# Kernel optimization log

Measured on AMD Instinct MI355X. Metric: run time of the kernel, lower is better.

## Reference

```python
import jax, jax.numpy as jnp
import numpy as np

D_MODEL = 1024
N_HEADS = 16
HEAD_DIM = D_MODEL // N_HEADS  # 64
BATCH = 2
SEQ = 2048
THETA = 10000.0


def _rope_tables(theta, d_k, max_seq_len):
    # matches RoPE.__init__: d = theta**(2*arange(d_k//2)/d_k); t = s / d
    inv = theta ** (2.0 * jnp.arange(0, d_k // 2, dtype=jnp.float32) / d_k)  # [d_k//2]
    s = jnp.arange(max_seq_len, dtype=jnp.float32)[:, None]  # [S,1]
    t = s / inv[None, :]  # [S, d_k//2]
    return jnp.sin(t), jnp.cos(t)


def setup_inputs() -> dict:
    key = jax.random.key(0)
    ks = jax.random.split(key, 5)
    std = np.sqrt(2.0 / (D_MODEL + D_MODEL))
    x = jax.random.normal(ks[0], (BATCH, SEQ, D_MODEL), dtype=jnp.float32)
    Wq = jax.random.normal(ks[1], (D_MODEL, D_MODEL), dtype=jnp.float32) * std
    Wk = jax.random.normal(ks[2], (D_MODEL, D_MODEL), dtype=jnp.float32) * std
    Wv = jax.random.normal(ks[3], (D_MODEL, D_MODEL), dtype=jnp.float32) * std
    Wo = jax.random.normal(ks[4], (D_MODEL, D_MODEL), dtype=jnp.float32) * std
    token_positions = jnp.arange(SEQ, dtype=jnp.int64)
    rope_sin, rope_cos = _rope_tables(THETA, HEAD_DIM, SEQ)
    return {"x": x, "token_positions": token_positions, "Wq": Wq, "Wk": Wk,
            "Wv": Wv, "Wo": Wo, "rope_sin": rope_sin, "rope_cos": rope_cos}


def _apply_rope(x, sin, cos):
    # x: [B, H, S, d_k]; sin/cos: [S, d_k//2] (gathered by token_positions)
    x1 = x[..., ::2]
    x2 = x[..., 1::2]
    x_even = x1 * cos - x2 * sin
    x_odd = x1 * sin + x2 * cos
    # interleave back: stack on last dim then flatten
    return jnp.stack([x_even, x_odd], axis=-1).reshape(x.shape)


def reference(x, token_positions, Wq, Wk, Wv, Wo, rope_sin, rope_cos):
    b, s, _ = x.shape
    h, d = N_HEADS, HEAD_DIM

    def proj(W):
        y = jnp.einsum('oi,bsi->bso', W, x)
        return y.reshape(b, s, h, d).transpose(0, 2, 1, 3)  # [b, h, s, d]

    q = proj(Wq)
    k = proj(Wk)
    v = proj(Wv)

    sin = rope_sin[token_positions]  # [s, d//2]
    cos = rope_cos[token_positions]
    q = _apply_rope(q, sin, cos)
    k = _apply_rope(k, sin, cos)

    # causal scaled-dot-product attention (FlashAttention.apply(..., True))
    scale = 1.0 / jnp.sqrt(jnp.asarray(d, dtype=x.dtype))
    scores = jnp.einsum('bhqd,bhkd->bhqk', q, k) * scale
    causal = jnp.tril(jnp.ones((s, s), dtype=bool))
    scores = jnp.where(causal, scores, jnp.finfo(x.dtype).min)
    attn = jax.nn.softmax(scores, axis=-1)
    out = jnp.einsum('bhqk,bhkd->bhqd', attn, v)  # [b, h, s, d]
    out = out.transpose(0, 2, 1, 3).reshape(b, s, h * d)
    return jnp.einsum('oi,bsi->bso', Wo, out)
```

## Files before the change

kernel.cpp:

```cpp
#include <hip/hip_runtime.h>
#include <hip/hip_bf16.h>
#include <math.h>

#define BATCH   2
#define S_LEN   2048
#define DM      1024
#define NH      16
#define HD      64
#define MROWS   4096

typedef __hip_bfloat16 bf16;
typedef __attribute__((ext_vector_type(8))) short short8;
typedef __attribute__((ext_vector_type(4))) float float4v;

#define QSCALE 0.18033688011112043f

#define WC_VM0   0x0F70
#define WC_VM4   0x0F74
#define WC_VM6   0x0F76
#define WC_LGKM0 0xC07F

__device__ __forceinline__ short f2s(float x) {
    union { bf16 h; short s; } u; u.h = __float2bfloat16(x); return u.s;
}
__device__ __forceinline__ short8 load8(const void* p) {
    return *reinterpret_cast<const short8*>(p);
}
__device__ __forceinline__ void cvt8(const float* g, bf16* d) {
    float4v a = *reinterpret_cast<const float4v*>(g);
    float4v b = *reinterpret_cast<const float4v*>(g + 4);
    short8 r;
    r[0] = f2s(a[0]); r[1] = f2s(a[1]); r[2] = f2s(a[2]); r[3] = f2s(a[3]);
    r[4] = f2s(b[0]); r[5] = f2s(b[1]); r[6] = f2s(b[2]); r[7] = f2s(b[3]);
    *reinterpret_cast<short8*>(d) = r;
}
__device__ __forceinline__ void gll16(const void* g, void* l) {
    __builtin_amdgcn_global_load_lds(
        (const __attribute__((address_space(1))) unsigned int*)g,
        (__attribute__((address_space(3))) unsigned int*)l,
        16, 0, 0);
}
__device__ __forceinline__ unsigned pack2(float a, float b) {
    union { float f; unsigned u; } ua, ub;
    ua.f = a; ub.f = b;
    return ((ua.u + 0x8000u) >> 16) | ((ub.u + 0x8000u) & 0xFFFF0000u);
}

__global__ __launch_bounds__(256) void cvt_kernel(const float* __restrict__ x,
                                                  const float* __restrict__ wq,
                                                  const float* __restrict__ wk,
                                                  const float* __restrict__ wv,
                                                  const float* __restrict__ wo,
                                                  bf16* __restrict__ xb,
                                                  bf16* __restrict__ wqb,
                                                  bf16* __restrict__ wkb,
                                                  bf16* __restrict__ wvb,
                                                  bf16* __restrict__ wob) {
    const size_t i = ((size_t)blockIdx.x * 256 + threadIdx.x) * 8;
    const size_t NX = (size_t)MROWS * DM;
    const size_t NW = (size_t)DM * DM;
    if (i < NX)                { cvt8(x  + i,               xb  + i); }
    else if (i < NX + NW)      { cvt8(wq + (i - NX),        wqb + (i - NX)); }
    else if (i < NX + 2 * NW)  { cvt8(wk + (i - NX - NW),   wkb + (i - NX - NW)); }
    else if (i < NX + 3 * NW)  { cvt8(wv + (i - NX - 2*NW), wvb + (i - NX - 2*NW)); }
    else                       { cvt8(wo + (i - NX - 3*NW), wob + (i - NX - 3*NW)); }
}

__global__ __launch_bounds__(256) void qkv_gemm(const bf16* __restrict__ A,
                                                const bf16* __restrict__ Wqb,
                                                const bf16* __restrict__ Wkb,
                                                const bf16* __restrict__ Wvb,
                                                bf16* __restrict__ Qb, bf16* __restrict__ Kb,
                                                bf16* __restrict__ Vtb,
                                                const float* __restrict__ rsin,
                                                const float* __restrict__ rcos) {
    __shared__ short As[2][128 * 32];
    __shared__ short Bs[2][128 * 32];

    const int j    = threadIdx.x;
    const int w    = j >> 6;
    const int lane = j & 63;
    const int quad = lane >> 4;
    const int lid  = lane & 15;
    const int wm   = w & 1, wn = w >> 1;

    const int mb  = blockIdx.x * 128;
    const int sel = blockIdx.y >> 3;
    const int nb  = (blockIdx.y & 7) * 128;
    const bf16* W = (sel == 0) ? Wqb : (sel == 1) ? Wkb : Wvb;

    int sOff[2];
#pragma unroll
    for (int i = 0; i < 2; ++i) {
        const int idx = (i * 4 + w) * 64 + lane;
        const int r = idx >> 2;
        const int c = (idx & 3) ^ (r & 3) ^ ((r >> 2) & 3);
        sOff[i] = r * DM + c * 8;
    }
    const bf16* baseA = A + (size_t)mb * DM;
    const bf16* baseB = W + (size_t)nb * DM;

#pragma unroll
    for (int i = 0; i < 2; ++i) gll16(baseA + sOff[i], &As[0][(i * 4 + w) * 512]);
#pragma unroll
    for (int i = 0; i < 2; ++i) gll16(baseB + sOff[i], &Bs[0][(i * 4 + w) * 512]);

    int aRd[4], bRd[4];
#pragma unroll
    for (int t = 0; t < 4; ++t) {
        const int ra = wm * 64 + t * 16 + lid;
        aRd[t] = ra * 32 + ((quad ^ (ra & 3) ^ ((ra >> 2) & 3)) * 8);
        const int rb = wn * 64 + t * 16 + lid;
        bRd[t] = rb * 32 + ((quad ^ (rb & 3) ^ ((rb >> 2) & 3)) * 8);
    }

    float4v acc[4][4] = {};
#pragma unroll 2
    for (int it = 0; it < 32; ++it) {
        __builtin_amdgcn_s_barrier();
        if (it < 31) {
            const int k0 = (it + 1) * 32, b = (it + 1) & 1;
#pragma unroll
            for (int i = 0; i < 2; ++i) gll16(baseA + k0 + sOff[i], &As[b][(i * 4 + w) * 512]);
#pragma unroll
            for (int i = 0; i < 2; ++i) gll16(baseB + k0 + sOff[i], &Bs[b][(i * 4 + w) * 512]);
            __builtin_amdgcn_s_waitcnt(WC_VM4);
        } else {
            __builtin_amdgcn_s_waitcnt(WC_VM0);
        }
        __builtin_amdgcn_s_barrier();

        const short* as = As[it & 1];
        const short* bs = Bs[it & 1];
        short8 af[4], bfr[4];
#pragma unroll
        for (int mt = 0; mt < 4; ++mt) af[mt] = load8(&as[aRd[mt]]);
#pragma unroll
        for (int nt = 0; nt < 4; ++nt) bfr[nt] = load8(&bs[bRd[nt]]);
#pragma unroll
        for (int mt = 0; mt < 4; ++mt)
#pragma unroll
            for (int nt = 0; nt < 4; ++nt)
                acc[mt][nt] = __builtin_amdgcn_mfma_f32_16x16x32_bf16(af[mt], bfr[nt], acc[mt][nt], 0, 0, 0);
    }

#pragma unroll
    for (int mt = 0; mt < 4; ++mt) {
#pragma unroll
        for (int nt = 0; nt < 4; ++nt) {
            const int n = nb + wn * 64 + nt * 16 + lid;
            const int h = n >> 6, d = n & 63;
#pragma unroll
            for (int r = 0; r < 4; ++r) {
                const int m = mb + wm * 64 + mt * 16 + quad * 4 + r;
                const int s = m & (S_LEN - 1), bi = m >> 11;
                float val = acc[mt][nt][r];
                if (sel == 0) val *= QSCALE;
                float par = __shfl_xor(val, 1, 64);
                if (sel == 2) {
                    Vtb[(((size_t)bi * NH + h) * HD + d) * S_LEN + s] = __float2bfloat16(val);
                } else {
                    const float sn = rsin[s * 32 + (d >> 1)];
                    const float cs = rcos[s * 32 + (d >> 1)];
                    const float v = ((d & 1) == 0) ? val * cs - par * sn
                                                   : par * sn + val * cs;
                    bf16* dst = (sel == 0) ? Qb : Kb;
                    dst[(((size_t)bi * NH + h) * S_LEN + s) * HD + d] = __float2bfloat16(v);
                }
            }
        }
    }
}

__global__ __launch_bounds__(256) void out_gemm(const bf16* __restrict__ A,
                                                const bf16* __restrict__ W,
                                                float* __restrict__ out) {
    __shared__ short As[2][128 * 64];
    __shared__ short Bs[2][64 * 64];

    const int j    = threadIdx.x;
    const int w    = j >> 6;
    const int lane = j & 63;
    const int quad = lane >> 4;
    const int lid  = lane & 15;

    const int mb = blockIdx.x * 128;
    const int nb = blockIdx.y * 64;

    int aOff[4], bOff[2];
#pragma unroll
    for (int i = 0; i < 4; ++i) {
        const int idx = (i * 4 + w) * 64 + lane;
        const int r = idx >> 3, c = (idx & 7) ^ (r & 7);
        aOff[i] = r * DM + c * 8;
    }
#pragma unroll
    for (int i = 0; i < 2; ++i) {
        const int idx = (i * 4 + w) * 64 + lane;
        const int r = idx >> 3, c = (idx & 7) ^ (r & 7);
        bOff[i] = r * DM + c * 8;
    }
    const bf16* baseA = A + (size_t)mb * DM;
    const bf16* baseB = W + (size_t)nb * DM;

#pragma unroll
    for (int i = 0; i < 4; ++i) gll16(baseA + aOff[i], &As[0][(i * 4 + w) * 512]);
#pragma unroll
    for (int i = 0; i < 2; ++i) gll16(baseB + bOff[i], &Bs[0][(i * 4 + w) * 512]);

    float4v acc[2][4] = {};
#pragma unroll 2
    for (int it = 0; it < 16; ++it) {
        __builtin_amdgcn_s_barrier();
        if (it < 15) {
            const int k0 = (it + 1) * 64, b = (it + 1) & 1;
#pragma unroll
            for (int i = 0; i < 4; ++i) gll16(baseA + k0 + aOff[i], &As[b][(i * 4 + w) * 512]);
#pragma unroll
            for (int i = 0; i < 2; ++i) gll16(baseB + k0 + bOff[i], &Bs[b][(i * 4 + w) * 512]);
            __builtin_amdgcn_s_waitcnt(WC_VM6);
        } else {
            __builtin_amdgcn_s_waitcnt(WC_VM0);
        }
        __builtin_amdgcn_s_barrier();

        const short* as = As[it & 1];
        const short* bs = Bs[it & 1];
#pragma unroll
        for (int ks = 0; ks < 2; ++ks) {
            short8 af[2], bfr[4];
#pragma unroll
            for (int mt = 0; mt < 2; ++mt)
                af[mt] = load8(&as[(w * 32 + mt * 16 + lid) * 64 + (((ks * 4 + quad) ^ (lid & 7)) * 8)]);
#pragma unroll
            for (int nt = 0; nt < 4; ++nt)
                bfr[nt] = load8(&bs[(nt * 16 + lid) * 64 + (((ks * 4 + quad) ^ (lid & 7)) * 8)]);
#pragma unroll
            for (int mt = 0; mt < 2; ++mt)
#pragma unroll
                for (int nt = 0; nt < 4; ++nt)
                    acc[mt][nt] = __builtin_amdgcn_mfma_f32_16x16x32_bf16(af[mt], bfr[nt], acc[mt][nt], 0, 0, 0);
        }
    }

#pragma unroll
    for (int mt = 0; mt < 2; ++mt)
#pragma unroll
        for (int nt = 0; nt < 4; ++nt) {
            const int n = nb + nt * 16 + lid;
#pragma unroll
            for (int r = 0; r < 4; ++r) {
                const int m = mb + w * 32 + mt * 16 + quad * 4 + r;
                out[(size_t)m * DM + n] = acc[mt][nt][r];
            }
        }
}

__global__ __launch_bounds__(256) void flash6(const bf16* __restrict__ Q,
                                              const bf16* __restrict__ K,
                                              const bf16* __restrict__ Vt,
                                              bf16* __restrict__ att) {
    __shared__ short Ks[128 * 64];
    __shared__ short Vs[64 * 128];
    __shared__ short Pb[128 * 128];

    const int j    = threadIdx.x;
    const int w    = j >> 6;
    const int lane = j & 63;
    const int quad = lane >> 4;
    const int lid  = lane & 15;
    const int bh   = blockIdx.x;
    const int by   = blockIdx.y;
    const int qt   = (by < 8) ? (15 - by) : (by - 8);
    const int bi   = bh >> 4, h = bh & 15;
    const int qb   = qt * 128;

    const size_t bh_off = (size_t)bh * S_LEN * HD;
    const bf16* Qp = Q + bh_off;
    const bf16* Kp = K + bh_off;
    const bf16* Vp = Vt + bh_off;

    short8 aQ[2][2];
#pragma unroll
    for (int mm = 0; mm < 2; ++mm)
#pragma unroll
        for (int kf = 0; kf < 2; ++kf)
            aQ[mm][kf] = load8(Qp + (size_t)(qb + w * 32 + mm * 16 + lid) * HD + kf * 32 + quad * 8);

    int kOff[4], vOff[4];
#pragma unroll
    for (int i = 0; i < 4; ++i) {
        const int idx = (i * 4 + w) * 64 + lane;
        const int kr = idx >> 3, kc = (idx & 7) ^ (kr & 7);
        kOff[i] = kr * HD + kc * 8;
        const int vr = idx >> 4, vc = (idx & 15) ^ (vr & 15);
        vOff[i] = vr * S_LEN + vc * 8;
    }

    float4v accO[2][4] = {};
    float4v accS[2] = {};
    short8 ones;
#pragma unroll
    for (int t = 0; t < 8; ++t) ones[t] = (short)0x3F80;

    short8 kReg[4], vReg[4];
#pragma unroll
    for (int i = 0; i < 4; ++i) kReg[i] = load8(Kp + kOff[i]);
#pragma unroll
    for (int i = 0; i < 4; ++i) vReg[i] = load8(Vp + vOff[i]);

    const int nkt = qt + 1;
    for (int kti = 0; kti < nkt; ++kti) {
        __builtin_amdgcn_s_barrier();
#pragma unroll
        for (int i = 0; i < 4; ++i)
            *reinterpret_cast<short8*>(&Ks[(i * 4 + w) * 512 + lane * 8]) = kReg[i];
#pragma unroll
        for (int i = 0; i < 4; ++i)
            *reinterpret_cast<short8*>(&Vs[(i * 4 + w) * 512 + lane * 8]) = vReg[i];
        if (kti + 1 < nkt) {
            const int ktn = (kti + 1) * 128;
#pragma unroll
            for (int i = 0; i < 4; ++i) kReg[i] = load8(Kp + (size_t)ktn * HD + kOff[i]);
#pragma unroll
            for (int i = 0; i < 4; ++i) vReg[i] = load8(Vp + ktn + vOff[i]);
        }
        __builtin_amdgcn_s_waitcnt(WC_LGKM0);
        __builtin_amdgcn_s_barrier();

        const int kt = kti * 128;
        const bool diag = (kti == nkt - 1);

#pragma unroll
        for (int nt = 0; nt < 8; ++nt) {
            const int krow = nt * 16 + lid;
            short8 aK0 = load8(&Ks[krow * 64 + ((quad       ^ (lid & 7)) * 8)]);
            short8 aK1 = load8(&Ks[krow * 64 + (((4 + quad) ^ (lid & 7)) * 8)]);
#pragma unroll
            for (int mm = 0; mm < 2; ++mm) {
                float4v z = {};
                z = __builtin_amdgcn_mfma_f32_16x16x32_bf16(aK0, aQ[mm][0], z, 0, 0, 0);
                z = __builtin_amdgcn_mfma_f32_16x16x32_bf16(aK1, aQ[mm][1], z, 0, 0, 0);
                if (diag) {
                    const int qcol = qb + w * 32 + mm * 16 + lid;
#pragma unroll
                    for (int r = 0; r < 4; ++r)
                        if (kt + nt * 16 + quad * 4 + r > qcol) z[r] = -1e30f;
                }
                const float p0 = __builtin_amdgcn_exp2f(z[0]);
                const float p1 = __builtin_amdgcn_exp2f(z[1]);
                const float p2 = __builtin_amdgcn_exp2f(z[2]);
                const float p3 = __builtin_amdgcn_exp2f(z[3]);
                const int qrow = w * 32 + mm * 16 + lid;
                const int unit = (nt * 4 + quad) ^ ((lid & 7) * 2);
                uint2 pkd; pkd.x = pack2(p0, p1); pkd.y = pack2(p2, p3);
                *reinterpret_cast<uint2*>(&Pb[qrow * 128 + unit * 4]) = pkd;
            }
        }

        short8 aP[2][4];
#pragma unroll
        for (int mm = 0; mm < 2; ++mm) {
            const int qrow = w * 32 + mm * 16 + lid;
#pragma unroll
            for (int g = 0; g < 4; ++g) {
                const int u = (g * 8 + quad * 2) ^ ((lid & 7) * 2);
                aP[mm][g] = load8(&Pb[qrow * 128 + u * 4]);
                accS[mm] = __builtin_amdgcn_mfma_f32_16x16x32_bf16(aP[mm][g], ones, accS[mm], 0, 0, 0);
            }
        }
#pragma unroll
        for (int dt = 0; dt < 4; ++dt) {
#pragma unroll
            for (int g = 0; g < 4; ++g) {
                short8 bV = load8(&Vs[(dt * 16 + lid) * 128 + (((g * 4 + quad) ^ lid) * 8)]);
#pragma unroll
                for (int mm = 0; mm < 2; ++mm)
                    accO[mm][dt] = __builtin_amdgcn_mfma_f32_16x16x32_bf16(aP[mm][g], bV, accO[mm][dt], 0, 0, 0);
            }
        }
    }

#pragma unroll
    for (int mm = 0; mm < 2; ++mm) {
#pragma unroll
        for (int r = 0; r < 4; ++r) {
            const float inv = 1.0f / accS[mm][r];
            const int q = qb + w * 32 + mm * 16 + quad * 4 + r;
#pragma unroll
            for (int dt = 0; dt < 4; ++dt) {
                const int d = dt * 16 + lid;
                att[((size_t)bi * S_LEN + q) * DM + h * HD + d] =
                    __float2bfloat16(accO[mm][dt][r] * inv);
            }
        }
    }
}

extern "C" void kernel_launch(void* const* d_in, const int* in_sizes, int n_in,
                              void* d_out, int out_size, void* d_ws, size_t ws_size,
                              hipStream_t stream) {
    const float* x    = (const float*)d_in[0];
    const float* Wq   = (const float*)d_in[2];
    const float* Wk   = (const float*)d_in[3];
    const float* Wv   = (const float*)d_in[4];
    const float* Wo   = (const float*)d_in[5];
    const float* rsin = (const float*)d_in[6];
    const float* rcos = (const float*)d_in[7];
    float* out = (float*)d_out;

    char* ws = (char*)d_ws;
    const size_t MB = 1024 * 1024;
    bf16* Qb  = (bf16*)(ws + 0 * MB);
    bf16* Kb  = (bf16*)(ws + 8 * MB);
    bf16* Vtb = (bf16*)(ws + 16 * MB);
    bf16* xb  = (bf16*)(ws + 24 * MB);
    bf16* Wqb = (bf16*)(ws + 32 * MB);
    bf16* Wkb = (bf16*)(ws + 34 * MB);
    bf16* Wvb = (bf16*)(ws + 36 * MB);
    bf16* Wob = (bf16*)(ws + 38 * MB);
    bf16* atb = xb;

    cvt_kernel<<<4096, 256, 0, stream>>>(x, Wq, Wk, Wv, Wo, xb, Wqb, Wkb, Wvb, Wob);
    qkv_gemm<<<dim3(MROWS / 128, 24), 256, 0, stream>>>(xb, Wqb, Wkb, Wvb, Qb, Kb, Vtb, rsin, rcos);
    flash6<<<dim3(BATCH * NH, 16), 256, 0, stream>>>(Qb, Kb, Vtb, atb);
    out_gemm<<<dim3(MROWS / 128, DM / 64), 256, 0, stream>>>(atb, Wob, out);
}
```

Measured before the change: 186.1 us.

## Triple-buffer LDS tiles in QKV and output GEMMs with two-stage prefetch

Both projection GEMMs move from double to triple LDS buffering, prefetching the K-tile two iterations ahead with adjusted vmcnt waits. The output GEMM also shrinks its K-step from 64 to 32, using the same XOR swizzle and precomputed read offsets as the QKV GEMM. The aim is to hide more global-load latency behind MFMA work. The cost is more barriers per K in the output GEMM, a rolling buffer index in place of a constant-folded parity, and dropping the unroll-2 pragma.

```diff
diff --git a/kernel.cpp b/kernel.cpp
--- a/kernel.cpp
+++ b/kernel.cpp
@@ -16,8 +16,10 @@
 #define QSCALE 0.18033688011112043f
 
 #define WC_VM0   0x0F70
+#define WC_VM3   0x0F73
 #define WC_VM4   0x0F74
 #define WC_VM6   0x0F76
+#define WC_VM8   0x0F78
 #define WC_LGKM0 0xC07F
 
 __device__ __forceinline__ short f2s(float x) {
@@ -74,8 +76,8 @@
                                                 bf16* __restrict__ Vtb,
                                                 const float* __restrict__ rsin,
                                                 const float* __restrict__ rcos) {
-    __shared__ short As[2][128 * 32];
-    __shared__ short Bs[2][128 * 32];
+    __shared__ short As[3][128 * 32];
+    __shared__ short Bs[3][128 * 32];
 
     const int j    = threadIdx.x;
     const int w    = j >> 6;
@@ -101,9 +103,12 @@
     const bf16* baseB = W + (size_t)nb * DM;
 
 #pragma unroll
-    for (int i = 0; i < 2; ++i) gll16(baseA + sOff[i], &As[0][(i * 4 + w) * 512]);
-#pragma unroll
-    for (int i = 0; i < 2; ++i) gll16(baseB + sOff[i], &Bs[0][(i * 4 + w) * 512]);
+    for (int t = 0; t < 2; ++t) {
+#pragma unroll
+        for (int i = 0; i < 2; ++i) gll16(baseA + t * 32 + sOff[i], &As[t][(i * 4 + w) * 512]);
+#pragma unroll
+        for (int i = 0; i < 2; ++i) gll16(baseB + t * 32 + sOff[i], &Bs[t][(i * 4 + w) * 512]);
+    }
 
     int aRd[4], bRd[4];
 #pragma unroll
@@ -115,23 +120,26 @@
     }
 
     float4v acc[4][4] = {};
-#pragma unroll 2
+    int buf = 0;
     for (int it = 0; it < 32; ++it) {
         __builtin_amdgcn_s_barrier();
-        if (it < 31) {
-            const int k0 = (it + 1) * 32, b = (it + 1) & 1;
+        if (it < 30) {
+            const int k0 = (it + 2) * 32;
+            const int b = (buf + 2 >= 3) ? buf - 1 : buf + 2;
 #pragma unroll
             for (int i = 0; i < 2; ++i) gll16(baseA + k0 + sOff[i], &As[b][(i * 4 + w) * 512]);
 #pragma unroll
             for (int i = 0; i < 2; ++i) gll16(baseB + k0 + sOff[i], &Bs[b][(i * 4 + w) * 512]);
+            __builtin_amdgcn_s_waitcnt(WC_VM8);
+        } else if (it == 30) {
             __builtin_amdgcn_s_waitcnt(WC_VM4);
         } else {
             __builtin_amdgcn_s_waitcnt(WC_VM0);
         }
         __builtin_amdgcn_s_barrier();
 
-        const short* as = As[it & 1];
-        const short* bs = Bs[it & 1];
+        const short* as = As[buf];
+        const short* bs = Bs[buf];
         short8 af[4], bfr[4];
 #pragma unroll
         for (int mt = 0; mt < 4; ++mt) af[mt] = load8(&as[aRd[mt]]);
@@ -142,6 +150,7 @@
 #pragma unroll
             for (int nt = 0; nt < 4; ++nt)
                 acc[mt][nt] = __builtin_amdgcn_mfma_f32_16x16x32_bf16(af[mt], bfr[nt], acc[mt][nt], 0, 0, 0);
+        buf = (buf == 2) ? 0 : buf + 1;
     }
 
 #pragma unroll
@@ -175,8 +184,8 @@
 __global__ __launch_bounds__(256) void out_gemm(const bf16* __restrict__ A,
                                                 const bf16* __restrict__ W,
                                                 float* __restrict__ out) {
-    __shared__ short As[2][128 * 64];
-    __shared__ short Bs[2][64 * 64];
+    __shared__ short As[3][128 * 32];
+    __shared__ short Bs[3][64 * 32];
 
     const int j    = threadIdx.x;
     const int w    = j >> 6;
@@ -187,60 +196,73 @@
     const int mb = blockIdx.x * 128;
     const int nb = blockIdx.y * 64;
 
-    int aOff[4], bOff[2];
-#pragma unroll
-    for (int i = 0; i < 4; ++i) {
-        const int idx = (i * 4 + w) * 64 + lane;
-        const int r = idx >> 3, c = (idx & 7) ^ (r & 7);
-        aOff[i] = r * DM + c * 8;
-    }
+    int aOff[2], bOff;
 #pragma unroll
     for (int i = 0; i < 2; ++i) {
         const int idx = (i * 4 + w) * 64 + lane;
-        const int r = idx >> 3, c = (idx & 7) ^ (r & 7);
-        bOff[i] = r * DM + c * 8;
+        const int r = idx >> 2;
+        const int c = (idx & 3) ^ (r & 3) ^ ((r >> 2) & 3);
+        aOff[i] = r * DM + c * 8;
+    }
+    {
+        const int idx = w * 64 + lane;
+        const int r = idx >> 2;
+        const int c = (idx & 3) ^ (r & 3) ^ ((r >> 2) & 3);
+        bOff = r * DM + c * 8;
     }
     const bf16* baseA = A + (size_t)mb * DM;
     const bf16* baseB = W + (size_t)nb * DM;
 
 #pragma unroll
-    for (int i = 0; i < 4; ++i) gll16(baseA + aOff[i], &As[0][(i * 4 + w) * 512]);
-#pragma unroll
-    for (int i = 0; i < 2; ++i) gll16(baseB + bOff[i], &Bs[0][(i * 4 + w) * 512]);
+    for (int t = 0; t < 2; ++t) {
+#pragma unroll
+        for (int i = 0; i < 2; ++i) gll16(baseA + t * 32 + aOff[i], &As[t][(i * 4 + w) * 512]);
+        gll16(baseB + t * 32 + bOff, &Bs[t][w * 512]);
+    }
+
+    int aRd[2], bRd[4];
+#pragma unroll
+    for (int t = 0; t < 2; ++t) {
+        const int ra = w * 32 + t * 16 + lid;
+        aRd[t] = ra * 32 + ((quad ^ (ra & 3) ^ ((ra >> 2) & 3)) * 8);
+    }
+#pragma unroll
+    for (int t = 0; t < 4; ++t) {
+        const int rb = t * 16 + lid;
+        bRd[t] = rb * 32 + ((quad ^ (rb & 3) ^ ((rb >> 2) & 3)) * 8);
+    }
 
     float4v acc[2][4] = {};
-#pragma unroll 2
-    for (int it = 0; it < 16; ++it) {
-        __builtin_amdgcn_s_barrier();
-        if (it < 15) {
-            const int k0 = (it + 1) * 64, b = (it + 1) & 1;
-#pragma unroll
-            for (int i = 0; i < 4; ++i) gll16(baseA + k0 + aOff[i], &As[b][(i * 4 + w) * 512]);
-#pragma unroll
-            for (int i = 0; i < 2; ++i) gll16(baseB + k0 + bOff[i], &Bs[b][(i * 4 + w) * 512]);
+    int buf = 0;
+    for (int it = 0; it < 32; ++it) {
+        __builtin_amdgcn_s_barrier();
+        if (it < 30) {
+            const int k0 = (it + 2) * 32;
+            const int b = (buf + 2 >= 3) ? buf - 1 : buf + 2;
+#pragma unroll
+            for (int i = 0; i < 2; ++i) gll16(baseA + k0 + aOff[i], &As[b][(i * 4 + w) * 512]);
+            gll16(baseB + k0 + bOff, &Bs[b][w * 512]);
             __builtin_amdgcn_s_waitcnt(WC_VM6);
+        } else if (it == 30) {
+            __builtin_amdgcn_s_waitcnt(WC_VM3);
         } else {
             __builtin_amdgcn_s_waitcnt(WC_VM0);
         }
         __builtin_amdgcn_s_barrier();
 
-        const short* as = As[it & 1];
-        const short* bs = Bs[it & 1];
-#pragma unroll
-        for (int ks = 0; ks < 2; ++ks) {
-            short8 af[2], bfr[4];
-#pragma unroll
-            for (int mt = 0; mt < 2; ++mt)
-                af[mt] = load8(&as[(w * 32 + mt * 16 + lid) * 64 + (((ks * 4 + quad) ^ (lid & 7)) * 8)]);
+        const short* as = As[buf];
+        const short* bs = Bs[buf];
+        short8 af[2], bfr[4];
+#pragma unroll
+        for (int mt = 0; mt < 2; ++mt) af[mt] = load8(&as[aRd[mt]]);
+#pragma unroll
+        for (int nt = 0; nt < 4; ++nt) bfr[nt] = load8(&bs[bRd[nt]]);
+#pragma unroll
+        for (int mt = 0; mt < 2; ++mt)
 #pragma unroll
             for (int nt = 0; nt < 4; ++nt)
-                bfr[nt] = load8(&bs[(nt * 16 + lid) * 64 + (((ks * 4 + quad) ^ (lid & 7)) * 8)]);
-#pragma unroll
-            for (int mt = 0; mt < 2; ++mt)
-#pragma unroll
-                for (int nt = 0; nt < 4; ++nt)
-                    acc[mt][nt] = __builtin_amdgcn_mfma_f32_16x16x32_bf16(af[mt], bfr[nt], acc[mt][nt], 0, 0, 0);
-        }
+                acc[mt][nt] = __builtin_amdgcn_mfma_f32_16x16x32_bf16(af[mt], bfr[nt], acc[mt][nt], 0, 0, 0);
+        buf = (buf == 2) ? 0 : buf + 1;
     }
 
 #pragma unroll
```

New measurement: 184.3 us. About the same (-1.0%).
